# Performance work log

Hardware: AMD Instinct MI355X
Metric: run time of the kernel (lower is better)

## Reference

```python
import jax, jax.numpy as jnp
import numpy as np

ALPHA = 0.05
EPS = 1e-5

N_NODES = 50000
N_MODAL = 4
D = 128
N_EDGES = 800000


def setup_inputs() -> dict:
    key = jax.random.key(0)
    k1, k2, k3, k4, k5 = jax.random.split(key, 5)
    multimodal = jax.random.normal(k1, (N_NODES, N_MODAL, D), dtype=jnp.float32)
    edge_src = jax.random.randint(k2, (N_EDGES,), 0, N_NODES, dtype=jnp.int32)
    edge_dst = jax.random.randint(k3, (N_EDGES,), 0, N_NODES, dtype=jnp.int32)
    edge_w = jax.random.uniform(k4, (N_EDGES,), dtype=jnp.float32)
    W = jax.random.normal(k5, (D, D), dtype=jnp.float32)
    gamma = jnp.ones((D,), dtype=jnp.float32)
    beta = jnp.zeros((D,), dtype=jnp.float32)
    return {"multimodal": multimodal, "edge_src": edge_src, "edge_dst": edge_dst,
            "edge_w": edge_w, "W": W, "gamma": gamma, "beta": beta}


def reference(multimodal, edge_src, edge_dst, edge_w, W, gamma, beta):
    N, M, Dd = multimodal.shape
    # sparse adj @ multimodal.reshape(N, M*D): gather src rows, weight, scatter-add to dst
    xf = multimodal.reshape(N, M * Dd)                       # [N, M*D]
    msgs = edge_w[:, None] * xf[edge_src]                    # [E, M*D]
    agg = jax.ops.segment_sum(msgs, edge_dst, num_segments=N)  # [N, M*D]
    # dense per-(node,modality) projection by W [D, D]
    out1 = (agg.reshape(N * M, Dd) @ W).reshape(N, M, Dd)
    # residual + LayerNorm over last dim (dropout is identity in eval)
    y = multimodal + ALPHA * out1
    mu = jnp.mean(y, axis=-1, keepdims=True)
    var = jnp.mean(jnp.square(y - mu), axis=-1, keepdims=True)
    out = (y - mu) * jax.lax.rsqrt(var + EPS) * gamma + beta
    return out
```

## Files before the change

kernel.cpp:

```cpp
#include <hip/hip_runtime.h>
#include <hip/hip_bf16.h>

#define D 128
#define MTOT 4
#define ALPHA 0.05f
#define LN_EPS 1e-5f

typedef __bf16 bf16x8_t __attribute__((ext_vector_type(8)));
typedef float f32x4_t __attribute__((ext_vector_type(4)));

union I4BF8 { int4 i; bf16x8_t v; ushort u[8]; };

__device__ __forceinline__ bool probe_f32(const void* gamma) {
    return *(const unsigned int*)gamma == 0x3F800000u;
}
__device__ __forceinline__ ushort f2bf(float f) {
    union { __hip_bfloat16 h; ushort u; } cv; cv.h = __float2bfloat16(f); return cv.u;
}
__device__ __forceinline__ float bf2f(ushort u) {
    union { ushort u; __hip_bfloat16 h; } cv; cv.u = u; return __bfloat162float(cv.h);
}

__global__ __launch_bounds__(256) void k_hist(const int* __restrict__ edst,
                                              unsigned* __restrict__ cnt, int E) {
    int e = blockIdx.x * 256 + threadIdx.x;
    if (e < E) atomicAdd(&cnt[edst[e]], 1u);
}

__global__ __launch_bounds__(256) void k_scan1(const unsigned* __restrict__ cnt,
                                               unsigned* __restrict__ offs,
                                               unsigned* __restrict__ bsum, int N) {
    __shared__ unsigned wsum[4];
    int t = threadIdx.x, lane = t & 63, wv = t >> 6;
    int base = blockIdx.x * 1024 + t * 4;
    unsigned v[4];
#pragma unroll
    for (int j = 0; j < 4; ++j) v[j] = (base + j < N) ? cnt[base + j] : 0u;
    unsigned ts = v[0] + v[1] + v[2] + v[3];
    unsigned sc = ts;
#pragma unroll
    for (int off = 1; off < 64; off <<= 1) {
        unsigned u = (unsigned)__shfl_up((int)sc, off, 64);
        if (lane >= off) sc += u;
    }
    if (lane == 63) wsum[wv] = sc;
    __syncthreads();
    if (t == 0) bsum[blockIdx.x] = wsum[0] + wsum[1] + wsum[2] + wsum[3];
    unsigned woff = 0;
    for (int w = 0; w < wv; ++w) woff += wsum[w];
    unsigned run = woff + sc - ts;
#pragma unroll
    for (int j = 0; j < 4; ++j) {
        if (base + j < N) offs[base + j] = run;
        run += v[j];
    }
}

__global__ __launch_bounds__(256) void k_scan23(unsigned* __restrict__ offs,
                                                const unsigned* __restrict__ bsum,
                                                unsigned* __restrict__ cursor,
                                                int N, int E) {
    __shared__ unsigned base_s;
    int i = blockIdx.x * 256 + threadIdx.x;
    int myblk = (blockIdx.x * 256) >> 10;
    if (threadIdx.x == 0) {
        unsigned s = 0;
        for (int b = 0; b < myblk; ++b) s += bsum[b];
        base_s = s;
    }
    __syncthreads();
    if (i < N) {
        unsigned o = offs[i] + base_s;
        offs[i] = o;
        cursor[i] = o;
    }
    if (i == 0) offs[N] = (unsigned)E;
}

__global__ __launch_bounds__(256) void k_reorder(const int* __restrict__ esrc,
                                                 const int* __restrict__ edst,
                                                 const void* __restrict__ ew,
                                                 const void* __restrict__ gamma,
                                                 unsigned* __restrict__ cursor,
                                                 int2* __restrict__ edges, int E) {
    bool f32 = probe_f32(gamma);
    int e = blockIdx.x * 256 + threadIdx.x;
    if (e >= E) return;
    float w = f32 ? ((const float*)ew)[e]
                  : __bfloat162float(((const __hip_bfloat16*)ew)[e]);
    unsigned pos = atomicAdd(&cursor[edst[e]], 1u);
    edges[pos] = make_int2(esrc[e], __float_as_int(w));
}

template <int MC>
__global__ __launch_bounds__(256) void k_cvt(const void* __restrict__ x,
                                             const void* __restrict__ gamma,
                                             ushort* __restrict__ xbf,
                                             int N, int mStart) {
    if (!probe_f32(gamma)) return;
    const int CPR = MC * D / 8;
    size_t total = (size_t)N * CPR;
    size_t stride = (size_t)gridDim.x * 256;
    for (size_t c = (size_t)blockIdx.x * 256 + threadIdx.x; c < total; c += stride) {
        int n = (int)(c / CPR);
        int fo = (int)(c % CPR) * 8;
        const float* xp = (const float*)x + ((size_t)n * MTOT + mStart) * D + fo;
        float4 a = *(const float4*)xp;
        float4 b = *(const float4*)(xp + 4);
        union { int4 i; ushort u[8]; } o;
        o.u[0] = f2bf(a.x); o.u[1] = f2bf(a.y);
        o.u[2] = f2bf(a.z); o.u[3] = f2bf(a.w);
        o.u[4] = f2bf(b.x); o.u[5] = f2bf(b.y);
        o.u[6] = f2bf(b.z); o.u[7] = f2bf(b.w);
        *(int4*)(xbf + c * 8) = o.i;
    }
}

template <int MC>
__global__ __launch_bounds__(256) void k_agg(const void* __restrict__ x,
                                             const ushort* __restrict__ xbf,
                                             const unsigned* __restrict__ offs,
                                             const int2* __restrict__ edges,
                                             const void* __restrict__ gamma,
                                             ushort* __restrict__ agg,
                                             int N, int mStart) {
    constexpr int FPL = MC * D / 64;
    bool f32 = probe_f32(gamma);
    int wid = (blockIdx.x * 256 + threadIdx.x) >> 6;
    int lane = threadIdx.x & 63;
    if (wid >= N) return;
    unsigned o0 = offs[wid], o1 = offs[wid + 1];
    float acc[FPL];
#pragma unroll
    for (int j = 0; j < FPL; ++j) acc[j] = 0.f;

    bool bfGather = !f32 || (xbf != nullptr);
    if (bfGather) {
        const ushort* src;
        size_t rstride;
        if (f32) { src = xbf;                                   rstride = MC * D; }
        else     { src = (const ushort*)x + (size_t)mStart * D; rstride = MTOT * D; }
        for (unsigned b = o0; b < o1; b += 64) {
            int2 ed = (b + (unsigned)lane < o1) ? edges[b + lane] : make_int2(0, 0);
            int n4 = (min((int)(o1 - b), 64) + 3) & ~3;
            for (int j = 0; j < n4; j += 4) {
                int s[4]; float w[4];
#pragma unroll
                for (int u = 0; u < 4; ++u) {
                    s[u] = __shfl(ed.x, j + u, 64);
                    w[u] = __int_as_float(__shfl(ed.y, j + u, 64));
                }
                if constexpr (FPL == 8) {
                    int4 r[4];
#pragma unroll
                    for (int u = 0; u < 4; ++u)
                        r[u] = *(const int4*)(src + (size_t)s[u] * rstride + lane * 8);
#pragma unroll
                    for (int u = 0; u < 4; ++u) {
                        union { int4 i; ushort us[8]; } c; c.i = r[u];
#pragma unroll
                        for (int k = 0; k < 8; ++k) acc[k] += w[u] * bf2f(c.us[k]);
                    }
                } else {
                    unsigned r[4];
#pragma unroll
                    for (int u = 0; u < 4; ++u)
                        r[u] = *(const unsigned*)(src + (size_t)s[u] * rstride + lane * 2);
#pragma unroll
                    for (int u = 0; u < 4; ++u) {
                        acc[0] += w[u] * bf2f((ushort)(r[u] & 0xFFFFu));
                        acc[1] += w[u] * bf2f((ushort)(r[u] >> 16));
                    }
                }
            }
        }
    } else {
        for (unsigned b = o0; b < o1; b += 64) {
            int2 ed = (b + (unsigned)lane < o1) ? edges[b + lane] : make_int2(0, 0);
            int n4 = (min((int)(o1 - b), 64) + 3) & ~3;
            for (int j = 0; j < n4; j += 4) {
                int s[4]; float w[4];
#pragma unroll
                for (int u = 0; u < 4; ++u) {
                    s[u] = __shfl(ed.x, j + u, 64);
                    w[u] = __int_as_float(__shfl(ed.y, j + u, 64));
                }
                if constexpr (FPL == 8) {
                    float4 ra[4], rb[4];
#pragma unroll
                    for (int u = 0; u < 4; ++u) {
                        const float* xp = (const float*)x +
                            ((size_t)s[u] * MTOT + mStart) * D + lane * 8;
                        ra[u] = *(const float4*)xp;
                        rb[u] = *(const float4*)(xp + 4);
                    }
#pragma unroll
                    for (int u = 0; u < 4; ++u) {
                        acc[0] += w[u] * ra[u].x; acc[1] += w[u] * ra[u].y;
                        acc[2] += w[u] * ra[u].z; acc[3] += w[u] * ra[u].w;
                        acc[4] += w[u] * rb[u].x; acc[5] += w[u] * rb[u].y;
                        acc[6] += w[u] * rb[u].z; acc[7] += w[u] * rb[u].w;
                    }
                } else {
                    float2 r[4];
#pragma unroll
                    for (int u = 0; u < 4; ++u)
                        r[u] = *(const float2*)((const float*)x +
                                 ((size_t)s[u] * MTOT + mStart) * D + lane * 2);
#pragma unroll
                    for (int u = 0; u < 4; ++u) {
                        acc[0] += w[u] * r[u].x;
                        acc[1] += w[u] * r[u].y;
                    }
                }
            }
        }
    }

    ushort* ap = agg + (size_t)wid * (MC * D) + lane * FPL;
    if constexpr (FPL == 8) {
        union { int4 i; ushort u[8]; } u;
#pragma unroll
        for (int k = 0; k < 8; ++k) u.u[k] = f2bf(acc[k]);
        *(int4*)ap = u.i;
    } else {
        union { unsigned i; ushort u[2]; } u;
        u.u[0] = f2bf(acc[0]); u.u[1] = f2bf(acc[1]);
        *(unsigned*)ap = u.i;
    }
}

template <int MC>
__global__ __launch_bounds__(256) void k_proj(const ushort* __restrict__ agg,
                                              const void* __restrict__ x,
                                              const void* __restrict__ W,
                                              const void* __restrict__ gamma,
                                              const void* __restrict__ beta,
                                              void* __restrict__ out,
                                              int R, int mStart) {
    bool f32 = probe_f32(gamma);
    __shared__ ushort Wf[4][8][64][8];
    __shared__ float yt[4][16][D + 4];
    __shared__ float gl[D], bl[D];

    int t = threadIdx.x, lane = t & 63, wv = t >> 6;

    if (t < D) {
        if (f32) {
            gl[t] = ((const float*)gamma)[t];
            bl[t] = ((const float*)beta)[t];
        } else {
            gl[t] = bf2f(((const ushort*)gamma)[t]);
            bl[t] = bf2f(((const ushort*)beta)[t]);
        }
    }
    {
        int kt = wv;
        int krow = (lane >> 4) * 8;
        int ncol = lane & 15;
        for (int ct = 0; ct < 8; ++ct) {
#pragma unroll
            for (int j = 0; j < 8; ++j) {
                int r = kt * 32 + krow + j, c = ct * 16 + ncol;
                ushort u = f32 ? f2bf(((const float*)W)[r * D + c])
                               : ((const ushort*)W)[r * D + c];
                Wf[kt][ct][lane][j] = u;
            }
        }
    }
    __syncthreads();

    int ntiles = R >> 4;
    int nwaves = gridDim.x * 4;
    for (int tile = blockIdx.x * 4 + wv; tile < ntiles; tile += nwaves) {
        int r0 = tile * 16;
        I4BF8 af[4];
        const ushort* ap = agg + ((size_t)(r0 + (lane & 15))) * D + (lane >> 4) * 8;
#pragma unroll
        for (int kt = 0; kt < 4; ++kt) af[kt].i = *(const int4*)(ap + kt * 32);

        f32x4_t accv[8];
#pragma unroll
        for (int ct = 0; ct < 8; ++ct) accv[ct] = (f32x4_t){0.f, 0.f, 0.f, 0.f};
#pragma unroll
        for (int kt = 0; kt < 4; ++kt) {
#pragma unroll
            for (int ct = 0; ct < 8; ++ct) {
                I4BF8 bfr;
                bfr.i = *(const int4*)&Wf[kt][ct][lane][0];
                accv[ct] = __builtin_amdgcn_mfma_f32_16x16x32_bf16(
                    af[kt].v, bfr.v, accv[ct], 0, 0, 0);
            }
        }
        int quad = lane >> 4, ccol = lane & 15;
#pragma unroll
        for (int ct = 0; ct < 8; ++ct)
#pragma unroll
            for (int rg = 0; rg < 4; ++rg)
                yt[wv][quad * 4 + rg][ct * 16 + ccol] = accv[ct][rg];

        int row = lane >> 2, q = lane & 3;
        int c0 = q * 32;
        int R_ = r0 + row;
        int xrow = (R_ / MC) * MTOT + mStart + (R_ % MC);

        float y[32];
        if (f32) {
            const float* xp = (const float*)x + (size_t)xrow * D + c0;
#pragma unroll
            for (int k = 0; k < 32; k += 4) {
                float4 f = *(const float4*)(xp + k);
                y[k] = f.x; y[k+1] = f.y; y[k+2] = f.z; y[k+3] = f.w;
            }
        } else {
            const ushort* xp = (const ushort*)x + (size_t)xrow * D + c0;
#pragma unroll
            for (int k = 0; k < 32; k += 8) {
                union { int4 i; ushort u[8]; } u;
                u.i = *(const int4*)(xp + k);
#pragma unroll
                for (int p = 0; p < 8; ++p) y[k + p] = bf2f(u.u[p]);
            }
        }
        float s = 0.f, sq = 0.f;
        const float* yr = &yt[wv][row][c0];
#pragma unroll
        for (int k = 0; k < 32; k += 4) {
            float4 a = *(const float4*)(yr + k);
            float v0 = y[k]   + ALPHA * a.x;
            float v1 = y[k+1] + ALPHA * a.y;
            float v2 = y[k+2] + ALPHA * a.z;
            float v3 = y[k+3] + ALPHA * a.w;
            y[k] = v0; y[k+1] = v1; y[k+2] = v2; y[k+3] = v3;
            s += v0 + v1 + v2 + v3;
            sq += v0*v0 + v1*v1 + v2*v2 + v3*v3;
        }
        s  += __shfl_xor(s, 1, 64);  s  += __shfl_xor(s, 2, 64);
        sq += __shfl_xor(sq, 1, 64); sq += __shfl_xor(sq, 2, 64);
        float mu = s * (1.0f / D);
        float var = sq * (1.0f / D) - mu * mu;
        float rstd = rsqrtf(var + LN_EPS);

        if (f32) {
            float* op = (float*)out + (size_t)xrow * D + c0;
#pragma unroll
            for (int k = 0; k < 32; k += 4) {
                float4 g = *(const float4*)&gl[c0 + k];
                float4 b = *(const float4*)&bl[c0 + k];
                float4 o;
                o.x = (y[k]   - mu) * rstd * g.x + b.x;
                o.y = (y[k+1] - mu) * rstd * g.y + b.y;
                o.z = (y[k+2] - mu) * rstd * g.z + b.z;
                o.w = (y[k+3] - mu) * rstd * g.w + b.w;
                *(float4*)(op + k) = o;
            }
        } else {
            ushort* op = (ushort*)out + (size_t)xrow * D + c0;
#pragma unroll
            for (int k = 0; k < 32; k += 8) {
                union { int4 i; ushort u[8]; } u;
#pragma unroll
                for (int p = 0; p < 8; ++p) {
                    float o = (y[k + p] - mu) * rstd * gl[c0 + k + p] + bl[c0 + k + p];
                    u.u[p] = f2bf(o);
                }
                *(int4*)(op + k) = u.i;
            }
        }
    }
}

extern "C" void kernel_launch(void* const* d_in, const int* in_sizes, int n_in,
                              void* d_out, int out_size, void* d_ws, size_t ws_size,
                              hipStream_t stream)
{
    const void* x     = d_in[0];
    const int*  esrc  = (const int*)d_in[1];
    const int*  edst  = (const int*)d_in[2];
    const void* ew    = d_in[3];
    const void* W     = d_in[4];
    const void* gamma = d_in[5];
    const void* beta  = d_in[6];

    int E   = in_sizes[1];
    int NMD = in_sizes[0];
    int N   = NMD / (MTOT * D);

    char* p = (char*)d_ws;
    auto alloc = [&](size_t bytes) {
        char* r = p; p += (bytes + 255) & ~(size_t)255; return r;
    };
    unsigned* cnt    = (unsigned*)alloc((size_t)N * 4);
    unsigned* offs   = (unsigned*)alloc((size_t)(N + 1) * 4);
    unsigned* bsum   = (unsigned*)alloc(256);
    unsigned* cursor = (unsigned*)alloc((size_t)N * 4);
    int2*     edges  = (int2*)alloc((size_t)E * 8);
    size_t fixedBytes = (size_t)(p - (char*)d_ws);

    size_t agg1 = (size_t)N * D * 2;
    size_t aggF = agg1 * MTOT;
    bool fullB = ws_size >= fixedBytes + aggF + 256;
    bool fullA = ws_size >= fixedBytes + 2 * aggF + 512;

    int nb = (N + 1023) / 1024;

    hipMemsetAsync(cnt, 0, (size_t)N * 4, stream);
    k_hist<<<(E + 255) / 256, 256, 0, stream>>>(edst, cnt, E);
    k_scan1<<<nb, 256, 0, stream>>>(cnt, offs, bsum, N);
    k_scan23<<<(N + 255) / 256, 256, 0, stream>>>(offs, bsum, cursor, N, E);
    k_reorder<<<(E + 255) / 256, 256, 0, stream>>>(esrc, edst, ew, gamma, cursor,
                                                   edges, E);

    int aggBlocks = (N * 64 + 255) / 256;
    if (fullB) {
        ushort* agg = (ushort*)alloc(aggF);
        ushort* xbf = fullA ? (ushort*)alloc(aggF) : nullptr;
        if (xbf)
            k_cvt<MTOT><<<2048, 256, 0, stream>>>(x, gamma, xbf, N, 0);
        k_agg<MTOT><<<aggBlocks, 256, 0, stream>>>(x, xbf, offs, edges, gamma,
                                                   agg, N, 0);
        int ntiles = (N * MTOT) / 16;
        k_proj<MTOT><<<(ntiles + 3) / 4, 256, 0, stream>>>(agg, x, W, gamma, beta,
                                                           d_out, N * MTOT, 0);
    } else {
        bool splitA = ws_size >= fixedBytes + 2 * agg1 + 512;
        ushort* agg = (ushort*)alloc(agg1);
        ushort* xbf = splitA ? (ushort*)alloc(agg1) : nullptr;
        for (int m = 0; m < MTOT; ++m) {
            if (xbf)
                k_cvt<1><<<1024, 256, 0, stream>>>(x, gamma, xbf, N, m);
            k_agg<1><<<aggBlocks, 256, 0, stream>>>(x, xbf, offs, edges, gamma,
                                                    agg, N, m);
            int ntiles = N / 16;
            k_proj<1><<<(ntiles + 3) / 4, 256, 0, stream>>>(agg, x, W, gamma, beta,
                                                            d_out, N, m);
        }
    }
}
```

Measured before the change: 538.9 us.

## Do LayerNorm epilogue in MFMA registers and cap projection grid

The projection kernel no longer stages the MFMA accumulators through a per-wave shared-memory tile. Each lane now applies the residual and LayerNorm directly on its accumulator fragment, reducing row statistics with 16-lane shuffles and keeping gamma/beta in registers. The grid is capped at 1024 persistent blocks so the W fragment load into shared memory is amortised across more tiles, and launch bounds request 4 blocks per CU. The trade-off is that global loads and stores of x and out become strided scalar accesses (16 lanes per contiguous 64B segment) instead of float4 vectors, and there are more shuffles per row.

```diff
diff --git a/kernel.cpp b/kernel.cpp
--- a/kernel.cpp
+++ b/kernel.cpp
@@ -231,29 +231,18 @@
 }
 
 template <int MC>
-__global__ __launch_bounds__(256) void k_proj(const ushort* __restrict__ agg,
-                                              const void* __restrict__ x,
-                                              const void* __restrict__ W,
-                                              const void* __restrict__ gamma,
-                                              const void* __restrict__ beta,
-                                              void* __restrict__ out,
-                                              int R, int mStart) {
+__global__ __launch_bounds__(256, 4) void k_proj(const ushort* __restrict__ agg,
+                                                 const void* __restrict__ x,
+                                                 const void* __restrict__ W,
+                                                 const void* __restrict__ gamma,
+                                                 const void* __restrict__ beta,
+                                                 void* __restrict__ out,
+                                                 int R, int mStart) {
     bool f32 = probe_f32(gamma);
     __shared__ ushort Wf[4][8][64][8];
-    __shared__ float yt[4][16][D + 4];
-    __shared__ float gl[D], bl[D];
 
     int t = threadIdx.x, lane = t & 63, wv = t >> 6;
 
-    if (t < D) {
-        if (f32) {
-            gl[t] = ((const float*)gamma)[t];
-            bl[t] = ((const float*)beta)[t];
-        } else {
-            gl[t] = bf2f(((const ushort*)gamma)[t]);
-            bl[t] = bf2f(((const ushort*)beta)[t]);
-        }
-    }
     {
         int kt = wv;
         int krow = (lane >> 4) * 8;
@@ -270,12 +259,27 @@
     }
     __syncthreads();
 
+    int quad = lane >> 4, cl = lane & 15;
+
+    float gl_r[8], bl_r[8];
+#pragma unroll
+    for (int ct = 0; ct < 8; ++ct) {
+        int c = ct * 16 + cl;
+        if (f32) {
+            gl_r[ct] = ((const float*)gamma)[c];
+            bl_r[ct] = ((const float*)beta)[c];
+        } else {
+            gl_r[ct] = bf2f(((const ushort*)gamma)[c]);
+            bl_r[ct] = bf2f(((const ushort*)beta)[c]);
+        }
+    }
+
     int ntiles = R >> 4;
     int nwaves = gridDim.x * 4;
     for (int tile = blockIdx.x * 4 + wv; tile < ntiles; tile += nwaves) {
         int r0 = tile * 16;
         I4BF8 af[4];
-        const ushort* ap = agg + ((size_t)(r0 + (lane & 15))) * D + (lane >> 4) * 8;
+        const ushort* ap = agg + ((size_t)(r0 + cl)) * D + quad * 8;
 #pragma unroll
         for (int kt = 0; kt < 4; ++kt) af[kt].i = *(const int4*)(ap + kt * 32);
 
@@ -292,79 +296,71 @@
                     af[kt].v, bfr.v, accv[ct], 0, 0, 0);
             }
         }
-        int quad = lane >> 4, ccol = lane & 15;
-#pragma unroll
-        for (int ct = 0; ct < 8; ++ct)
-#pragma unroll
-            for (int rg = 0; rg < 4; ++rg)
-                yt[wv][quad * 4 + rg][ct * 16 + ccol] = accv[ct][rg];
-
-        int row = lane >> 2, q = lane & 3;
-        int c0 = q * 32;
-        int R_ = r0 + row;
-        int xrow = (R_ / MC) * MTOT + mStart + (R_ % MC);
-
-        float y[32];
+
+        int xrow[4];
+#pragma unroll
+        for (int rg = 0; rg < 4; ++rg) {
+            int R_ = r0 + quad * 4 + rg;
+            xrow[rg] = (R_ / MC) * MTOT + mStart + (R_ % MC);
+        }
+
+        float s[4] = {0.f, 0.f, 0.f, 0.f}, sq[4] = {0.f, 0.f, 0.f, 0.f};
         if (f32) {
-            const float* xp = (const float*)x + (size_t)xrow * D + c0;
-#pragma unroll
-            for (int k = 0; k < 32; k += 4) {
-                float4 f = *(const float4*)(xp + k);
-                y[k] = f.x; y[k+1] = f.y; y[k+2] = f.z; y[k+3] = f.w;
+#pragma unroll
+            for (int rg = 0; rg < 4; ++rg) {
+                const float* xp = (const float*)x + (size_t)xrow[rg] * D + cl;
+#pragma unroll
+                for (int ct = 0; ct < 8; ++ct) {
+                    float y = xp[ct * 16] + ALPHA * accv[ct][rg];
+                    accv[ct][rg] = y;
+                    s[rg] += y; sq[rg] += y * y;
+                }
             }
         } else {
-            const ushort* xp = (const ushort*)x + (size_t)xrow * D + c0;
-#pragma unroll
-            for (int k = 0; k < 32; k += 8) {
-                union { int4 i; ushort u[8]; } u;
-                u.i = *(const int4*)(xp + k);
-#pragma unroll
-                for (int p = 0; p < 8; ++p) y[k + p] = bf2f(u.u[p]);
-            }
-        }
-        float s = 0.f, sq = 0.f;
-        const float* yr = &yt[wv][row][c0];
-#pragma unroll
-        for (int k = 0; k < 32; k += 4) {
-            float4 a = *(const float4*)(yr + k);
-            float v0 = y[k]   + ALPHA * a.x;
-            float v1 = y[k+1] + ALPHA * a.y;
-            float v2 = y[k+2] + ALPHA * a.z;
-            float v3 = y[k+3] + ALPHA * a.w;
-            y[k] = v0; y[k+1] = v1; y[k+2] = v2; y[k+3] = v3;
-            s += v0 + v1 + v2 + v3;
-            sq += v0*v0 + v1*v1 + v2*v2 + v3*v3;
-        }
-        s  += __shfl_xor(s, 1, 64);  s  += __shfl_xor(s, 2, 64);
-        sq += __shfl_xor(sq, 1, 64); sq += __shfl_xor(sq, 2, 64);
-        float mu = s * (1.0f / D);
-        float var = sq * (1.0f / D) - mu * mu;
-        float rstd = rsqrtf(var + LN_EPS);
+#pragma unroll
+            for (int rg = 0; rg < 4; ++rg) {
+                const ushort* xp = (const ushort*)x + (size_t)xrow[rg] * D + cl;
+#pragma unroll
+                for (int ct = 0; ct < 8; ++ct) {
+                    float y = bf2f(xp[ct * 16]) + ALPHA * accv[ct][rg];
+                    accv[ct][rg] = y;
+                    s[rg] += y; sq[rg] += y * y;
+                }
+            }
+        }
+#pragma unroll
+        for (int off = 1; off < 16; off <<= 1) {
+#pragma unroll
+            for (int rg = 0; rg < 4; ++rg) {
+                s[rg]  += __shfl_xor(s[rg],  off, 64);
+                sq[rg] += __shfl_xor(sq[rg], off, 64);
+            }
+        }
+        float mu[4], rstd[4];
+#pragma unroll
+        for (int rg = 0; rg < 4; ++rg) {
+            mu[rg] = s[rg] * (1.0f / D);
+            float var = sq[rg] * (1.0f / D) - mu[rg] * mu[rg];
+            rstd[rg] = rsqrtf(var + LN_EPS);
+        }
 
         if (f32) {
-            float* op = (float*)out + (size_t)xrow * D + c0;
-#pragma unroll
-            for (int k = 0; k < 32; k += 4) {
-                float4 g = *(const float4*)&gl[c0 + k];
-                float4 b = *(const float4*)&bl[c0 + k];
-                float4 o;
-                o.x = (y[k]   - mu) * rstd * g.x + b.x;
-                o.y = (y[k+1] - mu) * rstd * g.y + b.y;
-                o.z = (y[k+2] - mu) * rstd * g.z + b.z;
-                o.w = (y[k+3] - mu) * rstd * g.w + b.w;
-                *(float4*)(op + k) = o;
+#pragma unroll
+            for (int rg = 0; rg < 4; ++rg) {
+                float* op = (float*)out + (size_t)xrow[rg] * D + cl;
+#pragma unroll
+                for (int ct = 0; ct < 8; ++ct)
+                    op[ct * 16] = (accv[ct][rg] - mu[rg]) * rstd[rg] * gl_r[ct]
+                                  + bl_r[ct];
             }
         } else {
-            ushort* op = (ushort*)out + (size_t)xrow * D + c0;
-#pragma unroll
-            for (int k = 0; k < 32; k += 8) {
-                union { int4 i; ushort u[8]; } u;
-#pragma unroll
-                for (int p = 0; p < 8; ++p) {
-                    float o = (y[k + p] - mu) * rstd * gl[c0 + k + p] + bl[c0 + k + p];
-                    u.u[p] = f2bf(o);
-                }
-                *(int4*)(op + k) = u.i;
+#pragma unroll
+            for (int rg = 0; rg < 4; ++rg) {
+                ushort* op = (ushort*)out + (size_t)xrow[rg] * D + cl;
+#pragma unroll
+                for (int ct = 0; ct < 8; ++ct)
+                    op[ct * 16] = f2bf((accv[ct][rg] - mu[rg]) * rstd[rg] * gl_r[ct]
+                                       + bl_r[ct]);
             }
         }
     }
@@ -420,8 +416,10 @@
         k_agg<MTOT><<<aggBlocks, 256, 0, stream>>>(x, xbf, offs, edges, gamma,
                                                    agg, N, 0);
         int ntiles = (N * MTOT) / 16;
-        k_proj<MTOT><<<(ntiles + 3) / 4, 256, 0, stream>>>(agg, x, W, gamma, beta,
-                                                           d_out, N * MTOT, 0);
+        int pblocks = (ntiles + 3) / 4;
+        if (pblocks > 1024) pblocks = 1024;
+        k_proj<MTOT><<<pblocks, 256, 0, stream>>>(agg, x, W, gamma, beta,
+                                                  d_out, N * MTOT, 0);
     } else {
         bool splitA = ws_size >= fixedBytes + 2 * agg1 + 512;
         ushort* agg = (ushort*)alloc(agg1);
@@ -432,8 +430,10 @@
             k_agg<1><<<aggBlocks, 256, 0, stream>>>(x, xbf, offs, edges, gamma,
                                                     agg, N, m);
             int ntiles = N / 16;
-            k_proj<1><<<(ntiles + 3) / 4, 256, 0, stream>>>(agg, x, W, gamma, beta,
-                                                            d_out, N, m);
-        }
-    }
-}
+            int pblocks = (ntiles + 3) / 4;
+            if (pblocks > 1024) pblocks = 1024;
+            k_proj<1><<<pblocks, 256, 0, stream>>>(agg, x, W, gamma, beta,
+                                                   d_out, N, m);
+        }
+    }
+}
```

New measurement: 540.3 us. About the same (+0.3%).
